# Performance work log

Measured on AMD Instinct MI355X. Metric: run time of the kernel, lower is better.

The kernel has to match this reference:

```python
import jax, jax.numpy as jnp
import numpy as np

N = 50000        # num nodes
E = 800000       # num edges (before self-loops)
IN = 256         # in_channels
HID = 32         # hidden_channels per head
HEADS = 8
OUT = 64         # out_channels (layer 2, heads=1)
NEG_SLOPE = 0.2  # PyG GATConv default leaky_relu slope


def setup_inputs() -> dict:
    key = jax.random.key(0)
    ks = jax.random.split(key, 12)
    def rn(k, shape, scale=0.1):
        return jax.random.normal(k, shape, dtype=jnp.float32) * scale
    x = jax.random.normal(ks[0], (N, IN), dtype=jnp.float32)
    edge_index = jax.random.randint(ks[1], (2, E), 0, N, dtype=jnp.int64)
    return {
        "x": x,
        "edge_index": edge_index,
        # GATConv 1: in=256 -> 32 per head, 8 heads, concat
        "W1": rn(ks[2], (IN, HEADS * HID)),
        "att_src1": rn(ks[3], (HEADS, HID)),
        "att_dst1": rn(ks[4], (HEADS, HID)),
        "b1": jnp.zeros((HEADS * HID,), jnp.float32),
        # GATConv 2: in=256 -> 64, 1 head
        "W2": rn(ks[5], (HEADS * HID, OUT)),
        "att_src2": rn(ks[6], (1, OUT)),
        "att_dst2": rn(ks[7], (1, OUT)),
        "b2": jnp.zeros((OUT,), jnp.float32),
    }


def _gat_conv(x, src, dst, W, att_src, att_dst, bias, heads, out_ch):
    """PyG-style GATConv (add_self_loops already applied to src/dst).
    x: [N, F_in]; src/dst: [E']; returns [N, heads*out_ch] (concat)."""
    n = x.shape[0]
    h = (x @ W).reshape(n, heads, out_ch)                     # [N,H,F]
    a_src = jnp.einsum('nhf,hf->nh', h, att_src)              # [N,H]
    a_dst = jnp.einsum('nhf,hf->nh', h, att_dst)
    e = jax.nn.leaky_relu(a_src[src] + a_dst[dst], NEG_SLOPE)  # [E',H]
    # scatter-softmax over incoming edges of each dst node
    m = jax.ops.segment_max(e, dst, num_segments=n)            # [N,H]
    ex = jnp.exp(e - m[dst])
    denom = jax.ops.segment_sum(ex, dst, num_segments=n)       # [N,H]
    alpha = ex / denom[dst]                                    # [E',H]
    msg = alpha[:, :, None] * h[src]                           # [E',H,F]
    out = jax.ops.segment_sum(msg, dst, num_segments=n)        # [N,H,F]
    return out.reshape(n, heads * out_ch) + bias


def reference(x, edge_index, W1, att_src1, att_dst1, b1, W2, att_src2, att_dst2, b2):
    n = x.shape[0]
    loop = jnp.arange(n, dtype=edge_index.dtype)
    src = jnp.concatenate([edge_index[0], loop])  # add self-loops (PyG default)
    dst = jnp.concatenate([edge_index[1], loop])
    h = _gat_conv(x, src, dst, W1, att_src1, att_dst1, b1, HEADS, HID)
    h = jax.nn.relu(h)
    out = _gat_conv(h, src, dst, W2, att_src2, att_dst2, b2, 1, OUT)
    return out
```

## Files before the change

kernel.cpp:

```cpp
#include <hip/hip_runtime.h>
#include <hip/hip_bf16.h>


#define HEADS 8
#define HID 32
#define F1 256
#define F2 64
#define NEG_SLOPE 0.2f
#define CAP 128

typedef __attribute__((ext_vector_type(8))) short bf16x8;
typedef __attribute__((ext_vector_type(4))) float f32x4;
typedef __attribute__((ext_vector_type(8))) unsigned short u16x8;

__device__ __forceinline__ unsigned short f2b(float f) {
    union { float f; unsigned int i; } x; x.f = f;
    unsigned int r = x.i + 0x7fffu + ((x.i >> 16) & 1u);
    return (unsigned short)(r >> 16);
}
__device__ __forceinline__ float b2f(unsigned short u) {
    union { unsigned int i; float f; } x; x.i = ((unsigned int)u) << 16;
    return x.f;
}
__device__ __forceinline__ float leaky(float v) {
    return v > 0.f ? v : NEG_SLOPE * v;
}

__global__ void setup_kernel(const float* __restrict__ W1,
                             const float* __restrict__ W2,
                             unsigned short* __restrict__ W1T,
                             unsigned short* __restrict__ W2T,
                             int* __restrict__ cursor, int Nn) {
    const int i = blockIdx.x * 256 + threadIdx.x;
    if (i < F1 * F1) {
        const int k = i >> 8, n = i & (F1 - 1);
        W1T[(size_t)n * F1 + k] = f2b(W1[i]);
    } else if (i < F1 * F1 + F1 * F2) {
        const int j = i - F1 * F1;
        const int k = j >> 6, n = j & (F2 - 1);
        W2T[(size_t)n * F1 + k] = f2b(W2[j]);
    } else if (i < F1 * F1 + F1 * F2 + Nn) {
        cursor[i - F1 * F1 - F1 * F2] = 0;
    }
}

__global__ void scatter_kernel(const int* __restrict__ ei, int E,
                               int* __restrict__ cursor,
                               int* __restrict__ bucket) {
    const int e = blockIdx.x * blockDim.x + threadIdx.x;
    if (e >= E) return;
    const int d = ei[E + e];
    const int pos = atomicAdd(&cursor[d], 1);
    if (pos < CAP) bucket[(size_t)d * CAP + pos] = ei[e];
}

template<int BN, bool A_FP32, int OUT_MODE>
__global__ __launch_bounds__(256) void mfma_gemm(
        const void* __restrict__ A,
        const unsigned short* __restrict__ BT,
        void* __restrict__ C, int M, int N, int K) {
    constexpr int BM = 128, BK = 32;
    __shared__ unsigned short As[BM * BK];
    __shared__ unsigned short Bs[BN * BK];
    const int tid = threadIdx.x;
    const int wave = tid >> 6, lane = tid & 63;
    const int quad = lane >> 4, l16 = lane & 15;
    const int brow = blockIdx.x * BM;
    const int bcol = blockIdx.y * BN;

    constexpr int MI = (BN == 128) ? 4 : 2;
    constexpr int NJ = 4;
    const int wm = (BN == 128) ? (wave & 1) * 64 : wave * 32;
    const int wn = (BN == 128) ? (wave >> 1) * 64 : 0;

    f32x4 acc[MI][NJ] = {};

    for (int k0 = 0; k0 < K; k0 += BK) {
#pragma unroll
        for (int it = 0; it < (BM * BK) / (256 * 8); ++it) {
            const int idx = it * 256 + tid;
            const int r = idx >> 2;
            const int kk = (idx & 3) * 8;
            const int gr = brow + r;
            if (A_FP32) {
                const float* Af = (const float*)A;
                float4 a0 = make_float4(0.f, 0.f, 0.f, 0.f);
                float4 a1 = make_float4(0.f, 0.f, 0.f, 0.f);
                if (gr < M) {
                    a0 = *(const float4*)&Af[(size_t)gr * K + k0 + kk];
                    a1 = *(const float4*)&Af[(size_t)gr * K + k0 + kk + 4];
                }
                ushort4 lo, hi;
                lo.x = f2b(a0.x); lo.y = f2b(a0.y); lo.z = f2b(a0.z); lo.w = f2b(a0.w);
                hi.x = f2b(a1.x); hi.y = f2b(a1.y); hi.z = f2b(a1.z); hi.w = f2b(a1.w);
                *(ushort4*)&As[r * BK + kk] = lo;
                *(ushort4*)&As[r * BK + kk + 4] = hi;
            } else {
                const unsigned short* Ab = (const unsigned short*)A;
                uint4 v = make_uint4(0u, 0u, 0u, 0u);
                if (gr < M) v = *(const uint4*)&Ab[(size_t)gr * K + k0 + kk];
                *(uint4*)&As[r * BK + kk] = v;
            }
        }
#pragma unroll
        for (int it = 0; it < (BN * BK) / (256 * 8); ++it) {
            const int idx = it * 256 + tid;
            const int r = idx >> 2;
            const int kk = (idx & 3) * 8;
            const uint4 v = *(const uint4*)&BT[(size_t)(bcol + r) * K + k0 + kk];
            *(uint4*)&Bs[r * BK + kk] = v;
        }
        __syncthreads();
        bf16x8 af[MI], bfr[NJ];
#pragma unroll
        for (int i = 0; i < MI; ++i)
            af[i] = *(const bf16x8*)&As[(wm + i * 16 + l16) * BK + quad * 8];
#pragma unroll
        for (int j = 0; j < NJ; ++j)
            bfr[j] = *(const bf16x8*)&Bs[(wn + j * 16 + l16) * BK + quad * 8];
#pragma unroll
        for (int i = 0; i < MI; ++i)
#pragma unroll
            for (int j = 0; j < NJ; ++j)
                acc[i][j] = __builtin_amdgcn_mfma_f32_16x16x32_bf16(
                    af[i], bfr[j], acc[i][j], 0, 0, 0);
        __syncthreads();
    }
#pragma unroll
    for (int i = 0; i < MI; ++i) {
#pragma unroll
        for (int r = 0; r < 4; ++r) {
            const int row = brow + wm + i * 16 + quad * 4 + r;
            if (row >= M) continue;
#pragma unroll
            for (int j = 0; j < NJ; ++j) {
                const int col = bcol + wn + j * 16 + l16;
                const float v = acc[i][j][r];
                if (OUT_MODE == 0) {
                    ((float*)C)[(size_t)row * N + col] = v;
                } else if (OUT_MODE == 1) {
                    ((unsigned short*)C)[(size_t)row * N + col] = f2b(v);
                } else {
                    ((unsigned short*)C)[((size_t)(col >> 5) * M + row) * HID
                                         + (col & 31)] = f2b(v);
                }
            }
        }
    }
}

__global__ void att1_kernel(const unsigned short* __restrict__ h1hm,
                            const float* __restrict__ att_src,
                            const float* __restrict__ att_dst,
                            float* __restrict__ a_src,
                            float* __restrict__ a_dst, int Nn) {
    const int n = blockIdx.x * blockDim.x + threadIdx.x;
    const int h = blockIdx.y;
    if (n >= Nn) return;
    const unsigned short* hp = h1hm + ((size_t)h * Nn + n) * HID;
    const float* as = att_src + h * HID;
    const float* ad = att_dst + h * HID;
    float s = 0.f, d = 0.f;
#pragma unroll
    for (int f = 0; f < HID; ++f) {
        const float v = b2f(hp[f]);
        s += v * as[f];
        d += v * ad[f];
    }
    a_src[(size_t)h * Nn + n] = s;
    a_dst[(size_t)h * Nn + n] = d;
}

__global__ void att2_kernel(const unsigned short* __restrict__ h2b,
                            const float* __restrict__ att_src,
                            const float* __restrict__ att_dst,
                            float* __restrict__ a_src,
                            float* __restrict__ a_dst, int Nn) {
    const int n = blockIdx.x * blockDim.x + threadIdx.x;
    if (n >= Nn) return;
    const unsigned short* hp = h2b + (size_t)n * F2;
    float s = 0.f, d = 0.f;
#pragma unroll
    for (int f = 0; f < F2; ++f) {
        const float v = b2f(hp[f]);
        s += v * att_src[f];
        d += v * att_dst[f];
    }
    a_src[n] = s;
    a_dst[n] = d;
}

__global__ __launch_bounds__(256) void gather1_kernel(
        const int* __restrict__ cursor, const int* __restrict__ bucket,
        const float* __restrict__ a_src, const float* __restrict__ a_dst,
        const unsigned short* __restrict__ h1hm, const float* __restrict__ b1,
        unsigned short* __restrict__ out1b, int Nn) {
    const int h = blockIdx.x & 7;
    const int lane = threadIdx.x & 63;
    const int wv = threadIdx.x >> 6;
    const int sub = lane >> 2;
    const int cl  = lane & 3;
    const int d = (blockIdx.x >> 3) * 64 + wv * 16 + sub;
    if (d >= Nn) return;

    const unsigned short* hh = h1hm + (size_t)h * Nn * HID;
    const float* asrc = a_src + (size_t)h * Nn;
    const float adst = a_dst[(size_t)h * Nn + d];

    float denom, acc[8];
    {
        const float w = __expf(leaky(asrc[d] + adst));
        const u16x8 v = *(const u16x8*)&hh[(size_t)d * HID + cl * 8];
        denom = w;
#pragma unroll
        for (int q = 0; q < 8; ++q) acc[q] = w * b2f(v[q]);
    }
    const int base = d * CAP;
    const int cnt = min(cursor[d], CAP);
    for (int i = 0; i < cnt; i += 4) {
        const int4 s4 = *(const int4*)&bucket[base + i];
        int s[4];
        bool ok[4];
        s[0] = s4.x; s[1] = s4.y; s[2] = s4.z; s[3] = s4.w;
#pragma unroll
        for (int j = 0; j < 4; ++j) {
            ok[j] = (i + j) < cnt;
            s[j] = ok[j] ? s[j] : d;
        }
        float e[4];
#pragma unroll
        for (int j = 0; j < 4; ++j) e[j] = asrc[s[j]];
        u16x8 vv[4];
#pragma unroll
        for (int j = 0; j < 4; ++j)
            vv[j] = *(const u16x8*)&hh[(size_t)s[j] * HID + cl * 8];
#pragma unroll
        for (int j = 0; j < 4; ++j) {
            float w = __expf(leaky(e[j] + adst));
            w = ok[j] ? w : 0.f;
            denom += w;
#pragma unroll
            for (int q = 0; q < 8; ++q) acc[q] += w * b2f(vv[j][q]);
        }
    }
    const float inv = 1.f / denom;
    const int c = h * HID + cl * 8;
    u16x8 o;
#pragma unroll
    for (int q = 0; q < 8; ++q)
        o[q] = f2b(fmaxf(acc[q] * inv + b1[c + q], 0.f));
    *(u16x8*)&out1b[(size_t)d * F1 + c] = o;
}

__global__ __launch_bounds__(256) void gather2_kernel(
        const int* __restrict__ cursor, const int* __restrict__ bucket,
        const float* __restrict__ a_src, const float* __restrict__ a_dst,
        const unsigned short* __restrict__ h2b, const float* __restrict__ b2,
        float* __restrict__ out, int Nn) {
    const int lane = threadIdx.x & 63;
    const int sub  = lane >> 4;
    const int l    = lane & 15;
    int d = blockIdx.x * 16 + (threadIdx.x >> 6) * 4 + sub;
    const bool valid = d < Nn;
    if (!valid) d = Nn - 1;
    const int c = l * 4;

    const float adst = a_dst[d];
    float a0, a1, a2, a3, denom;
    {
        const float w = __expf(leaky(a_src[d] + adst));
        const ushort4 v = *(const ushort4*)&h2b[(size_t)d * F2 + c];
        denom = w;
        a0 = w * b2f(v.x); a1 = w * b2f(v.y);
        a2 = w * b2f(v.z); a3 = w * b2f(v.w);
    }
    const int base = d * CAP;
    const int cnt = min(cursor[d], CAP);
    for (int i = 0; i < cnt; i += 4) {
        const int4 s4 = *(const int4*)&bucket[base + i];
        int s[4] = { s4.x, s4.y, s4.z, s4.w };
        float e[4];
        ushort4 vv[4];
#pragma unroll
        for (int jj = 0; jj < 4; ++jj) {
            const bool ok = (i + jj) < cnt;
            const int ss = ok ? s[jj] : d;
            s[jj] = ok ? 1 : -1;
            e[jj] = a_src[ss];
            vv[jj] = *(const ushort4*)&h2b[(size_t)ss * F2 + c];
        }
#pragma unroll
        for (int jj = 0; jj < 4; ++jj) {
            float w = __expf(leaky(e[jj] + adst));
            w = s[jj] < 0 ? 0.f : w;
            denom += w;
            a0 += w * b2f(vv[jj].x); a1 += w * b2f(vv[jj].y);
            a2 += w * b2f(vv[jj].z); a3 += w * b2f(vv[jj].w);
        }
    }
    if (valid) {
        const float inv = 1.f / denom;
        float4 o;
        o.x = a0 * inv + b2[c + 0];
        o.y = a1 * inv + b2[c + 1];
        o.z = a2 * inv + b2[c + 2];
        o.w = a3 * inv + b2[c + 3];
        *(float4*)&out[(size_t)d * F2 + c] = o;
    }
}

extern "C" void kernel_launch(void* const* d_in, const int* in_sizes, int n_in,
                              void* d_out, int out_size, void* d_ws, size_t ws_size,
                              hipStream_t stream) {
    const float* x        = (const float*)d_in[0];
    const int*   ei       = (const int*)d_in[1];
    const float* W1       = (const float*)d_in[2];
    const float* att_src1 = (const float*)d_in[3];
    const float* att_dst1 = (const float*)d_in[4];
    const float* b1       = (const float*)d_in[5];
    const float* W2       = (const float*)d_in[6];
    const float* att_src2 = (const float*)d_in[7];
    const float* att_dst2 = (const float*)d_in[8];
    const float* b2       = (const float*)d_in[9];
    float* out = (float*)d_out;

    const int Nn = in_sizes[0] / F1;
    const int E  = in_sizes[1] / 2;

    char* p = (char*)d_ws;
    unsigned short* h1hm  = (unsigned short*)p; p += (size_t)Nn * F1 * 2;
    unsigned short* out1b = (unsigned short*)p; p += (size_t)Nn * F1 * 2;
    unsigned short* W1T   = (unsigned short*)p; p += (size_t)F1 * F1 * 2;
    unsigned short* W2T   = (unsigned short*)p; p += (size_t)F2 * F1 * 2;
    unsigned short* h2b   = (unsigned short*)p; p += (size_t)Nn * F2 * 2;
    float* a_src1 = (float*)p; p += (size_t)Nn * HEADS * 4;
    float* a_dst1 = (float*)p; p += (size_t)Nn * HEADS * 4;
    float* a_src2 = (float*)p; p += (size_t)Nn * 4;
    float* a_dst2 = (float*)p; p += (size_t)Nn * 4;
    int* cursor  = (int*)p; p += (size_t)Nn * 4;
    int* bucket  = (int*)p; p += (size_t)Nn * CAP * 4;

    {
        const int total = F1 * F1 + F1 * F2 + Nn;
        setup_kernel<<<(total + 255) / 256, 256, 0, stream>>>(
            W1, W2, W1T, W2T, cursor, Nn);
    }
    scatter_kernel<<<(E + 255) / 256, 256, 0, stream>>>(ei, E, cursor, bucket);

    {
        dim3 grid((Nn + 127) / 128, F1 / 128);
        mfma_gemm<128, true, 2><<<grid, 256, 0, stream>>>(
            x, W1T, h1hm, Nn, F1, F1);
    }
    {
        dim3 grid((Nn + 255) / 256, HEADS);
        att1_kernel<<<grid, 256, 0, stream>>>(
            h1hm, att_src1, att_dst1, a_src1, a_dst1, Nn);
    }
    gather1_kernel<<<((Nn + 63) / 64) * 8, 256, 0, stream>>>(
        cursor, bucket, a_src1, a_dst1, h1hm, b1, out1b, Nn);

    {
        dim3 grid((Nn + 127) / 128, F2 / 64);
        mfma_gemm<64, false, 1><<<grid, 256, 0, stream>>>(
            out1b, W2T, h2b, Nn, F2, F1);
    }
    att2_kernel<<<(Nn + 255) / 256, 256, 0, stream>>>(
        h2b, att_src2, att_dst2, a_src2, a_dst2, Nn);
    gather2_kernel<<<(Nn + 15) / 16, 256, 0, stream>>>(
        cursor, bucket, a_src2, a_dst2, h2b, b2, out, Nn);
}
```

Before: 301.7 us.

## Fuse attention-score dot products into GEMM epilogues and use nontemporal memory ops

The separate att1 and att2 kernels are removed. The a_src/a_dst dot products are now computed inside the MFMA GEMM epilogue from the fp32 accumulators, using cross-lane shuffles over each head's 32 columns. This removes two launches and a re-read of the bf16 h1/h2 features, and the scores now come from unrounded fp32 values. Separately, bucket stores and loads, out1b, and the final output use nontemporal builtins to reduce cache pollution. The cost is extra shuffle work and register pressure in the GEMM epilogue.

```diff
diff --git a/kernel.cpp b/kernel.cpp
--- a/kernel.cpp
+++ b/kernel.cpp
@@ -12,6 +12,8 @@
 typedef __attribute__((ext_vector_type(8))) short bf16x8;
 typedef __attribute__((ext_vector_type(4))) float f32x4;
 typedef __attribute__((ext_vector_type(8))) unsigned short u16x8;
+typedef __attribute__((ext_vector_type(4))) unsigned short u16x4;
+typedef __attribute__((ext_vector_type(4))) int i32x4;
 
 __device__ __forceinline__ unsigned short f2b(float f) {
     union { float f; unsigned int i; } x; x.f = f;
@@ -51,14 +53,18 @@
     if (e >= E) return;
     const int d = ei[E + e];
     const int pos = atomicAdd(&cursor[d], 1);
-    if (pos < CAP) bucket[(size_t)d * CAP + pos] = ei[e];
-}
-
-template<int BN, bool A_FP32, int OUT_MODE>
+    if (pos < CAP)
+        __builtin_nontemporal_store(ei[e], &bucket[(size_t)d * CAP + pos]);
+}
+
+template<int BN, bool A_FP32, int OUT_MODE, int FUSE>
 __global__ __launch_bounds__(256) void mfma_gemm(
         const void* __restrict__ A,
         const unsigned short* __restrict__ BT,
-        void* __restrict__ C, int M, int N, int K) {
+        void* __restrict__ C,
+        const float* __restrict__ attS, const float* __restrict__ attD,
+        float* __restrict__ aS, float* __restrict__ aD,
+        int M, int N, int K) {
     constexpr int BM = 128, BK = 32;
     __shared__ unsigned short As[BM * BK];
     __shared__ unsigned short Bs[BN * BK];
@@ -136,9 +142,7 @@
             for (int j = 0; j < NJ; ++j) {
                 const int col = bcol + wn + j * 16 + l16;
                 const float v = acc[i][j][r];
-                if (OUT_MODE == 0) {
-                    ((float*)C)[(size_t)row * N + col] = v;
-                } else if (OUT_MODE == 1) {
+                if (OUT_MODE == 1) {
                     ((unsigned short*)C)[(size_t)row * N + col] = f2b(v);
                 } else {
                     ((unsigned short*)C)[((size_t)(col >> 5) * M + row) * HID
@@ -147,47 +151,66 @@
             }
         }
     }
-}
-
-__global__ void att1_kernel(const unsigned short* __restrict__ h1hm,
-                            const float* __restrict__ att_src,
-                            const float* __restrict__ att_dst,
-                            float* __restrict__ a_src,
-                            float* __restrict__ a_dst, int Nn) {
-    const int n = blockIdx.x * blockDim.x + threadIdx.x;
-    const int h = blockIdx.y;
-    if (n >= Nn) return;
-    const unsigned short* hp = h1hm + ((size_t)h * Nn + n) * HID;
-    const float* as = att_src + h * HID;
-    const float* ad = att_dst + h * HID;
-    float s = 0.f, d = 0.f;
-#pragma unroll
-    for (int f = 0; f < HID; ++f) {
-        const float v = b2f(hp[f]);
-        s += v * as[f];
-        d += v * ad[f];
-    }
-    a_src[(size_t)h * Nn + n] = s;
-    a_dst[(size_t)h * Nn + n] = d;
-}
-
-__global__ void att2_kernel(const unsigned short* __restrict__ h2b,
-                            const float* __restrict__ att_src,
-                            const float* __restrict__ att_dst,
-                            float* __restrict__ a_src,
-                            float* __restrict__ a_dst, int Nn) {
-    const int n = blockIdx.x * blockDim.x + threadIdx.x;
-    if (n >= Nn) return;
-    const unsigned short* hp = h2b + (size_t)n * F2;
-    float s = 0.f, d = 0.f;
-#pragma unroll
-    for (int f = 0; f < F2; ++f) {
-        const float v = b2f(hp[f]);
-        s += v * att_src[f];
-        d += v * att_dst[f];
-    }
-    a_src[n] = s;
-    a_dst[n] = d;
+    if (FUSE == 1) {
+        const int head0 = (bcol + wn) >> 5;
+        const float aS0 = attS[head0 * 32 + l16];
+        const float aS1 = attS[head0 * 32 + 16 + l16];
+        const float aS2 = attS[(head0 + 1) * 32 + l16];
+        const float aS3 = attS[(head0 + 1) * 32 + 16 + l16];
+        const float aD0 = attD[head0 * 32 + l16];
+        const float aD1 = attD[head0 * 32 + 16 + l16];
+        const float aD2 = attD[(head0 + 1) * 32 + l16];
+        const float aD3 = attD[(head0 + 1) * 32 + 16 + l16];
+#pragma unroll
+        for (int i = 0; i < MI; ++i) {
+#pragma unroll
+            for (int r = 0; r < 4; ++r) {
+                float s0 = acc[i][0][r] * aS0 + acc[i][1][r] * aS1;
+                float s1 = acc[i][2][r] * aS2 + acc[i][3][r] * aS3;
+                float d0 = acc[i][0][r] * aD0 + acc[i][1][r] * aD1;
+                float d1 = acc[i][2][r] * aD2 + acc[i][3][r] * aD3;
+#pragma unroll
+                for (int off = 1; off < 16; off <<= 1) {
+                    s0 += __shfl_xor(s0, off, 64);
+                    s1 += __shfl_xor(s1, off, 64);
+                    d0 += __shfl_xor(d0, off, 64);
+                    d1 += __shfl_xor(d1, off, 64);
+                }
+                const int row = brow + wm + i * 16 + quad * 4 + r;
+                if (l16 == 0 && row < M) {
+                    aS[(size_t)head0 * M + row] = s0;
+                    aS[(size_t)(head0 + 1) * M + row] = s1;
+                    aD[(size_t)head0 * M + row] = d0;
+                    aD[(size_t)(head0 + 1) * M + row] = d1;
+                }
+            }
+        }
+    } else if (FUSE == 2) {
+        const float aSj0 = attS[l16],      aDj0 = attD[l16];
+        const float aSj1 = attS[16 + l16], aDj1 = attD[16 + l16];
+        const float aSj2 = attS[32 + l16], aDj2 = attD[32 + l16];
+        const float aSj3 = attS[48 + l16], aDj3 = attD[48 + l16];
+#pragma unroll
+        for (int i = 0; i < MI; ++i) {
+#pragma unroll
+            for (int r = 0; r < 4; ++r) {
+                float s = acc[i][0][r] * aSj0 + acc[i][1][r] * aSj1
+                        + acc[i][2][r] * aSj2 + acc[i][3][r] * aSj3;
+                float d = acc[i][0][r] * aDj0 + acc[i][1][r] * aDj1
+                        + acc[i][2][r] * aDj2 + acc[i][3][r] * aDj3;
+#pragma unroll
+                for (int off = 1; off < 16; off <<= 1) {
+                    s += __shfl_xor(s, off, 64);
+                    d += __shfl_xor(d, off, 64);
+                }
+                const int row = brow + wm + i * 16 + quad * 4 + r;
+                if (l16 == 0 && row < M) {
+                    aS[row] = s;
+                    aD[row] = d;
+                }
+            }
+        }
+    }
 }
 
 __global__ __launch_bounds__(256) void gather1_kernel(
@@ -218,14 +241,14 @@
     const int base = d * CAP;
     const int cnt = min(cursor[d], CAP);
     for (int i = 0; i < cnt; i += 4) {
-        const int4 s4 = *(const int4*)&bucket[base + i];
+        const i32x4 s4 =
+            __builtin_nontemporal_load((const i32x4*)&bucket[base + i]);
         int s[4];
         bool ok[4];
-        s[0] = s4.x; s[1] = s4.y; s[2] = s4.z; s[3] = s4.w;
 #pragma unroll
         for (int j = 0; j < 4; ++j) {
             ok[j] = (i + j) < cnt;
-            s[j] = ok[j] ? s[j] : d;
+            s[j] = ok[j] ? s4[j] : d;
         }
         float e[4];
 #pragma unroll
@@ -249,7 +272,7 @@
 #pragma unroll
     for (int q = 0; q < 8; ++q)
         o[q] = f2b(fmaxf(acc[q] * inv + b1[c + q], 0.f));
-    *(u16x8*)&out1b[(size_t)d * F1 + c] = o;
+    __builtin_nontemporal_store(o, (u16x8*)&out1b[(size_t)d * F1 + c]);
 }
 
 __global__ __launch_bounds__(256) void gather2_kernel(
@@ -277,22 +300,22 @@
     const int base = d * CAP;
     const int cnt = min(cursor[d], CAP);
     for (int i = 0; i < cnt; i += 4) {
-        const int4 s4 = *(const int4*)&bucket[base + i];
-        int s[4] = { s4.x, s4.y, s4.z, s4.w };
+        const i32x4 s4 =
+            __builtin_nontemporal_load((const i32x4*)&bucket[base + i]);
         float e[4];
         ushort4 vv[4];
+        bool ok[4];
 #pragma unroll
         for (int jj = 0; jj < 4; ++jj) {
-            const bool ok = (i + jj) < cnt;
-            const int ss = ok ? s[jj] : d;
-            s[jj] = ok ? 1 : -1;
+            ok[jj] = (i + jj) < cnt;
+            const int ss = ok[jj] ? s4[jj] : d;
             e[jj] = a_src[ss];
             vv[jj] = *(const ushort4*)&h2b[(size_t)ss * F2 + c];
         }
 #pragma unroll
         for (int jj = 0; jj < 4; ++jj) {
             float w = __expf(leaky(e[jj] + adst));
-            w = s[jj] < 0 ? 0.f : w;
+            w = ok[jj] ? w : 0.f;
             denom += w;
             a0 += w * b2f(vv[jj].x); a1 += w * b2f(vv[jj].y);
             a2 += w * b2f(vv[jj].z); a3 += w * b2f(vv[jj].w);
@@ -300,12 +323,12 @@
     }
     if (valid) {
         const float inv = 1.f / denom;
-        float4 o;
-        o.x = a0 * inv + b2[c + 0];
-        o.y = a1 * inv + b2[c + 1];
-        o.z = a2 * inv + b2[c + 2];
-        o.w = a3 * inv + b2[c + 3];
-        *(float4*)&out[(size_t)d * F2 + c] = o;
+        f32x4 o;
+        o[0] = a0 * inv + b2[c + 0];
+        o[1] = a1 * inv + b2[c + 1];
+        o[2] = a2 * inv + b2[c + 2];
+        o[3] = a3 * inv + b2[c + 3];
+        __builtin_nontemporal_store(o, (f32x4*)&out[(size_t)d * F2 + c]);
     }
 }
 
@@ -349,24 +372,17 @@
 
     {
         dim3 grid((Nn + 127) / 128, F1 / 128);
-        mfma_gemm<128, true, 2><<<grid, 256, 0, stream>>>(
-            x, W1T, h1hm, Nn, F1, F1);
-    }
-    {
-        dim3 grid((Nn + 255) / 256, HEADS);
-        att1_kernel<<<grid, 256, 0, stream>>>(
-            h1hm, att_src1, att_dst1, a_src1, a_dst1, Nn);
+        mfma_gemm<128, true, 2, 1><<<grid, 256, 0, stream>>>(
+            x, W1T, h1hm, att_src1, att_dst1, a_src1, a_dst1, Nn, F1, F1);
     }
     gather1_kernel<<<((Nn + 63) / 64) * 8, 256, 0, stream>>>(
         cursor, bucket, a_src1, a_dst1, h1hm, b1, out1b, Nn);
 
     {
         dim3 grid((Nn + 127) / 128, F2 / 64);
-        mfma_gemm<64, false, 1><<<grid, 256, 0, stream>>>(
-            out1b, W2T, h2b, Nn, F2, F1);
-    }
-    att2_kernel<<<(Nn + 255) / 256, 256, 0, stream>>>(
-        h2b, att_src2, att_dst2, a_src2, a_dst2, Nn);
+        mfma_gemm<64, false, 1, 2><<<grid, 256, 0, stream>>>(
+            out1b, W2T, h2b, att_src2, att_dst2, a_src2, a_dst2, Nn, F2, F1);
+    }
     gather2_kernel<<<(Nn + 15) / 16, 256, 0, stream>>>(
         cursor, bucket, a_src2, a_dst2, h2b, b2, out, Nn);
 }
```

Measured after the change: 350.5 us. 1.16x slower.
